# Optimization experiments

Measured on AMD Instinct MI355X. Metric: run time of the kernel, lower is better.

The kernel has to match this reference:

```python
import jax, jax.numpy as jnp
import numpy as np

TOTAL_INSTANCES = 131072
NUM_BAGS = 64
FEATURE_DIM = 512
HIDDEN_DIM = 256


def setup_inputs() -> dict:
    key = jax.random.key(0)
    k1, k2, k3 = jax.random.split(key, 3)
    instance_features = jax.random.normal(k1, (TOTAL_INSTANCES, FEATURE_DIM), dtype=jnp.float32)
    # Equal-sized bags (sum(bag_sizes) == TOTAL_INSTANCES); the reference handles ragged sizes too.
    bag_sizes = jnp.full((NUM_BAGS,), TOTAL_INSTANCES // NUM_BAGS, dtype=jnp.int32)
    W1 = jax.random.normal(k2, (FEATURE_DIM, HIDDEN_DIM), dtype=jnp.float32) * (1.0 / np.sqrt(FEATURE_DIM))
    b1 = jnp.zeros((HIDDEN_DIM,), dtype=jnp.float32)
    W2 = jax.random.normal(k3, (HIDDEN_DIM, 1), dtype=jnp.float32) * (1.0 / np.sqrt(HIDDEN_DIM))
    b2 = jnp.zeros((1,), dtype=jnp.float32)
    return {
        "instance_features": instance_features,
        "bag_sizes": bag_sizes,
        "W1": W1,
        "b1": b1,
        "W2": W2,
        "b2": b2,
    }


def reference(instance_features, bag_sizes, W1, b1, W2, b2):
    # Attention MLP: Linear -> Tanh -> Linear  => scores [T, 1]
    scores = jnp.tanh(instance_features @ W1 + b1) @ W2 + b2
    # Faithful to the original: softmax over dim=0 GLOBALLY across all instances.
    weights = jax.nn.softmax(scores, axis=0)  # [T, 1]
    T = instance_features.shape[0]
    B = bag_sizes.shape[0]
    # Ragged bag membership: instance i belongs to the first bag whose cumulative
    # size exceeds i.
    offsets = jnp.cumsum(bag_sizes)  # [B]
    seg_ids = jnp.searchsorted(offsets, jnp.arange(T), side="right")  # [T]
    # Per-bag weighted sum of instances: [B, feature_dim]
    return jax.ops.segment_sum(instance_features * weights, seg_ids, num_segments=B)
```

## Files before the change

kernel.cpp:

```cpp
#include <hip/hip_runtime.h>

typedef __attribute__((ext_vector_type(8))) short short8;
typedef __attribute__((ext_vector_type(4))) float floatx4;

#define FDIM 512
#define HDIM 256

__device__ __forceinline__ unsigned short f2bf(float f) {
  unsigned int u = __float_as_uint(f);
  u += 0x7fffu + ((u >> 16) & 1u);
  return (unsigned short)(u >> 16);
}

__device__ __forceinline__ short8 pack2(float4 a, float4 b) {
  short8 r;
  r[0] = (short)f2bf(a.x); r[1] = (short)f2bf(a.y);
  r[2] = (short)f2bf(a.z); r[3] = (short)f2bf(a.w);
  r[4] = (short)f2bf(b.x); r[5] = (short)f2bf(b.y);
  r[6] = (short)f2bf(b.z); r[7] = (short)f2bf(b.w);
  return r;
}

__device__ __forceinline__ float fast_tanh(float x) {
  x = fminf(15.0f, fmaxf(-15.0f, x));
  float e = __expf(2.0f * x);
  return (e - 1.0f) / (e + 1.0f);
}

__device__ __forceinline__ void gload_lds16(const void* g, void* l) {
  __builtin_amdgcn_global_load_lds(
      (const __attribute__((address_space(1))) unsigned int*)g,
      (__attribute__((address_space(3))) unsigned int*)l, 16, 0, 0);
}

__global__ void __launch_bounds__(256)
k0_pack_w1(const float* __restrict__ W1, unsigned short* __restrict__ W1B,
           float* __restrict__ out) {
  int tid = threadIdx.x;
  int idx = blockIdx.x * 256 + tid;
  if (blockIdx.x < 128) out[blockIdx.x * 256 + tid] = 0.0f;
  int k = idx >> 8;
  int n = idx & 255;
  int s = k >> 5, r = k & 31, oct = r >> 3, e = r & 7;
  W1B[s * 8192 + oct * 2048 + n * 8 + e] = f2bf(W1[idx]);
}

__global__ void __launch_bounds__(512)
k1_fused(const float* __restrict__ X,
         const unsigned short* __restrict__ W1B,
         const float* __restrict__ b1,
         const float* __restrict__ W2,
         const int* __restrict__ bag_sizes,
         int nbags,
         float* __restrict__ out,
         float* __restrict__ partials) {
  __shared__ __align__(16) unsigned char smem[163840];
  unsigned short* As  = (unsigned short*)smem;
  unsigned short* Bs0 = (unsigned short*)(smem + 131072);
  unsigned short* Bs1 = (unsigned short*)(smem + 147456);
  float* scpart = (float*)(smem + 131072);
  float* es_s   = (float*)(smem + 131072 + 2048);
  float* wsum_s = (float*)(smem + 131072 + 2560);

  const int tid  = threadIdx.x;
  const int wid  = tid >> 6;
  const int lane = tid & 63;
  const int l15  = lane & 15;
  const int l4   = lane >> 4;
  const int wr   = wid >> 2;
  const int wn   = wid & 3;
  const long row0 = (long)blockIdx.x * 128;

  floatx4 acc[4][4];
  #pragma unroll
  for (int m = 0; m < 4; m++)
    #pragma unroll
    for (int n = 0; n < 4; n++)
      acc[m][n] = (floatx4){0.f, 0.f, 0.f, 0.f};

  const int arow = tid >> 2;
  const int aoct = tid & 3;
  const float* xsrc = X + (row0 + arow) * FDIM + aoct * 8;

  float4 va0, va1, vb0, vb1;
  { const float4* pp = (const float4*)xsrc;        va0 = pp[0]; va1 = pp[1]; }
  { const float4* pp = (const float4*)(xsrc + 32); vb0 = pp[0]; vb1 = pp[1]; }
  #pragma unroll
  for (int i = 0; i < 2; ++i)
    gload_lds16(W1B + (i * 512 + tid) * 8, Bs0 + (i * 512 + wid * 64) * 8);

  for (int t = 0; t < 16; ++t) {
    unsigned short* Bcur = (t & 1) ? Bs1 : Bs0;
    {
      int slot = t * 4 + aoct;
      unsigned short* dst = As + (slot * 128 + (arow ^ (slot & 7))) * 8;
      if ((t & 1) == 0) *(short8*)dst = pack2(va0, va1);
      else              *(short8*)dst = pack2(vb0, vb1);
    }
    __syncthreads();
    if (t < 14) {
      const float4* pp = (const float4*)(xsrc + (t + 2) * 32);
      if ((t & 1) == 0) { va0 = pp[0]; va1 = pp[1]; }
      else              { vb0 = pp[0]; vb1 = pp[1]; }
    }
    if (t < 15) {
      unsigned short* Bn = (t & 1) ? Bs0 : Bs1;
      #pragma unroll
      for (int i = 0; i < 2; ++i)
        gload_lds16(W1B + (t + 1) * 8192 + (i * 512 + tid) * 8,
                    Bn + (i * 512 + wid * 64) * 8);
    }
    const int slotc = t * 4 + l4;
    const int gg = slotc & 7;
    short8 af[4];
    #pragma unroll
    for (int m = 0; m < 4; ++m)
      af[m] = *(const short8*)(As + (slotc * 128 + ((wr * 64 + m * 16 + l15) ^ gg)) * 8);
    #pragma unroll
    for (int n = 0; n < 4; ++n) {
      short8 bfr = *(const short8*)(Bcur + (l4 * 256 + wn * 64 + n * 16 + l15) * 8);
      #pragma unroll
      for (int m = 0; m < 4; ++m)
        acc[m][n] = __builtin_amdgcn_mfma_f32_16x16x32_bf16(af[m], bfr, acc[m][n], 0, 0, 0);
    }
  }

  float rowacc[16];
  #pragma unroll
  for (int i = 0; i < 16; i++) rowacc[i] = 0.f;
  #pragma unroll
  for (int n = 0; n < 4; n++) {
    int c = wn * 64 + n * 16 + l15;
    float b1c = b1[c];
    float w2c = W2[c];
    #pragma unroll
    for (int m = 0; m < 4; m++)
      #pragma unroll
      for (int j = 0; j < 4; j++) {
        float h = fast_tanh(acc[m][n][j] + b1c);
        rowacc[m * 4 + j] = fmaf(h, w2c, rowacc[m * 4 + j]);
      }
  }
  #pragma unroll
  for (int i = 0; i < 16; i++) {
    float v = rowacc[i];
    v += __shfl_xor(v, 1, 64);
    v += __shfl_xor(v, 2, 64);
    v += __shfl_xor(v, 4, 64);
    v += __shfl_xor(v, 8, 64);
    rowacc[i] = v;
  }
  if (l15 == 0) {
    #pragma unroll
    for (int m = 0; m < 4; m++)
      #pragma unroll
      for (int j = 0; j < 4; j++)
        scpart[wn * 128 + wr * 64 + m * 16 + l4 * 4 + j] = rowacc[m * 4 + j];
  }
  __syncthreads();

  if (tid < 128) {
    float sv = scpart[0 * 128 + tid] + scpart[1 * 128 + tid] +
               scpart[2 * 128 + tid] + scpart[3 * 128 + tid];
    float ev = __expf(sv);
    es_s[tid] = ev;
    float v = ev;
    v += __shfl_xor(v, 1, 64);
    v += __shfl_xor(v, 2, 64);
    v += __shfl_xor(v, 4, 64);
    v += __shfl_xor(v, 8, 64);
    v += __shfl_xor(v, 16, 64);
    v += __shfl_xor(v, 32, 64);
    if (lane == 0) wsum_s[wid] = v;
  }
  __syncthreads();
  if (tid == 0) partials[blockIdx.x] = wsum_s[0] + wsum_s[1];

  const int s  = tid >> 3;
  const int p  = tid & 7;
  const int gp = s & 7;
  const int fbase = (s >> 2) * 32 + (s & 3) * 8;
  const unsigned short* abase = As + s * 1024;

  int bag = 0; long cum = 0;
  while (bag + 1 < nbags && cum + (long)bag_sizes[bag] <= row0) {
    cum += bag_sizes[bag]; ++bag;
  }
  long bagEnd = cum + (long)bag_sizes[bag];

  int rs = 0;
  while (rs < 128) {
    int se = (int)(bagEnd - row0 < 128 ? bagEnd - row0 : 128);
    float pa[8];
    #pragma unroll
    for (int e = 0; e < 8; ++e) pa[e] = 0.f;
    #pragma unroll
    for (int j = 0; j < 16; ++j) {
      int r = p + 8 * j;
      if (r >= rs && r < se) {
        float w = es_s[r];
        short8 xv = *(const short8*)(abase + ((r ^ gp) * 8));
        const unsigned int* ui = (const unsigned int*)&xv;
        #pragma unroll
        for (int d = 0; d < 4; ++d) {
          float xlo = __uint_as_float(ui[d] << 16);
          float xhi = __uint_as_float(ui[d] & 0xffff0000u);
          pa[2 * d]     = fmaf(xlo, w, pa[2 * d]);
          pa[2 * d + 1] = fmaf(xhi, w, pa[2 * d + 1]);
        }
      }
    }
    #pragma unroll
    for (int e = 0; e < 8; ++e) {
      pa[e] += __shfl_xor(pa[e], 1, 64);
      pa[e] += __shfl_xor(pa[e], 2, 64);
      pa[e] += __shfl_xor(pa[e], 4, 64);
    }
    if (p == 0 && se > rs) {
      float* op = out + (long)bag * FDIM + fbase;
      #pragma unroll
      for (int e = 0; e < 8; ++e) atomicAdd(op + e, pa[e]);
    }
    rs = se;
    if (rs < 128) {
      ++bag;
      if (bag >= nbags) { bagEnd = row0 + 128; bag = nbags - 1; }
      else bagEnd += (long)bag_sizes[bag];
    }
  }
}

__global__ void __launch_bounds__(256)
k2_scale(const float* __restrict__ partials, int nparts, float* __restrict__ out) {
  __shared__ float wred[4];
  int tid = threadIdx.x;
  float sL = 0.f;
  for (int j = tid; j < nparts; j += 256) sL += partials[j];
  #pragma unroll
  for (int m = 1; m < 64; m <<= 1) sL += __shfl_xor(sL, m, 64);
  if ((tid & 63) == 0) wred[tid >> 6] = sL;
  __syncthreads();
  float invZ = 1.0f / (wred[0] + wred[1] + wred[2] + wred[3]);
  int i = blockIdx.x * 256 + tid;
  out[i] = out[i] * invZ;
}

extern "C" void kernel_launch(void* const* d_in, const int* in_sizes, int n_in,
                              void* d_out, int out_size, void* d_ws, size_t ws_size,
                              hipStream_t stream) {
  const float* X         = (const float*)d_in[0];
  const int*   bag_sizes = (const int*)d_in[1];
  const float* W1        = (const float*)d_in[2];
  const float* b1        = (const float*)d_in[3];
  const float* W2        = (const float*)d_in[4];
  float* out = (float*)d_out;

  const int T     = in_sizes[0] / FDIM;
  const int nbags = in_sizes[1];
  const int nblk  = T / 128;

  char* ws = (char*)d_ws;
  unsigned short* W1B = (unsigned short*)ws;
  float* partials = (float*)(ws + 262144);

  hipLaunchKernelGGL(k0_pack_w1, dim3(512), dim3(256), 0, stream, W1, W1B, out);
  hipLaunchKernelGGL(k1_fused, dim3(nblk), dim3(512), 0, stream,
                     X, W1B, b1, W2, bag_sizes, nbags, out, partials);
  hipLaunchKernelGGL(k2_scale, dim3((nbags * FDIM) / 256), dim3(256), 0, stream,
                     partials, nblk, out);
}
```

Measured before the change: 119.0 us.

## Hand-schedule X prefetch and W1 LDS loads with explicit vmcnt waits

Replaces the compiler-generated global loads of X with inline-asm dwordx4 loads and uses explicit s_waitcnt vmcnt counts plus raw s_barrier in place of __syncthreads. Each step waits only for the loads it needs, so X prefetches and W1 global-to-LDS transfers can stay in flight across the barrier. The K loop is also fully unrolled. The cost is a fragile dependence on exact load issue order: a wrong vmcnt value would read stale registers or LDS.

```diff
diff --git a/kernel.cpp b/kernel.cpp
--- a/kernel.cpp
+++ b/kernel.cpp
@@ -12,12 +12,12 @@
   return (unsigned short)(u >> 16);
 }
 
-__device__ __forceinline__ short8 pack2(float4 a, float4 b) {
+__device__ __forceinline__ short8 pack2(floatx4 a, floatx4 b) {
   short8 r;
-  r[0] = (short)f2bf(a.x); r[1] = (short)f2bf(a.y);
-  r[2] = (short)f2bf(a.z); r[3] = (short)f2bf(a.w);
-  r[4] = (short)f2bf(b.x); r[5] = (short)f2bf(b.y);
-  r[6] = (short)f2bf(b.z); r[7] = (short)f2bf(b.w);
+  r[0] = (short)f2bf(a[0]); r[1] = (short)f2bf(a[1]);
+  r[2] = (short)f2bf(a[2]); r[3] = (short)f2bf(a[3]);
+  r[4] = (short)f2bf(b[0]); r[5] = (short)f2bf(b[1]);
+  r[6] = (short)f2bf(b[2]); r[7] = (short)f2bf(b[3]);
   return r;
 }
 
@@ -32,6 +32,14 @@
       (const __attribute__((address_space(1))) unsigned int*)g,
       (__attribute__((address_space(3))) unsigned int*)l, 16, 0, 0);
 }
+
+#define GLOAD_SET(r0, r1, p)                                                   \
+  do {                                                                         \
+    asm volatile("global_load_dwordx4 %0, %1, off"                             \
+                 : "=v"(r0) : "v"(p) : "memory");                              \
+    asm volatile("global_load_dwordx4 %0, %1, off offset:16"                   \
+                 : "=v"(r1) : "v"(p) : "memory");                              \
+  } while (0)
 
 __global__ void __launch_bounds__(256)
 k0_pack_w1(const float* __restrict__ W1, unsigned short* __restrict__ W1B,
@@ -82,33 +90,41 @@
   const int aoct = tid & 3;
   const float* xsrc = X + (row0 + arow) * FDIM + aoct * 8;
 
-  float4 va0, va1, vb0, vb1;
-  { const float4* pp = (const float4*)xsrc;        va0 = pp[0]; va1 = pp[1]; }
-  { const float4* pp = (const float4*)(xsrc + 32); vb0 = pp[0]; vb1 = pp[1]; }
+  floatx4 va0, va1, vb0, vb1;
+
+  GLOAD_SET(va0, va1, xsrc);
   #pragma unroll
   for (int i = 0; i < 2; ++i)
     gload_lds16(W1B + (i * 512 + tid) * 8, Bs0 + (i * 512 + wid * 64) * 8);
-
+  GLOAD_SET(vb0, vb1, xsrc + 32);
+
+  #pragma unroll
   for (int t = 0; t < 16; ++t) {
     unsigned short* Bcur = (t & 1) ? Bs1 : Bs0;
+    if (t < 15) asm volatile("s_waitcnt vmcnt(4)" ::: "memory");
+    else        asm volatile("s_waitcnt vmcnt(2)" ::: "memory");
+    __builtin_amdgcn_sched_barrier(0);
     {
+      short8 a = ((t & 1) == 0) ? pack2(va0, va1) : pack2(vb0, vb1);
       int slot = t * 4 + aoct;
-      unsigned short* dst = As + (slot * 128 + (arow ^ (slot & 7))) * 8;
-      if ((t & 1) == 0) *(short8*)dst = pack2(va0, va1);
-      else              *(short8*)dst = pack2(vb0, vb1);
-    }
-    __syncthreads();
-    if (t < 14) {
-      const float4* pp = (const float4*)(xsrc + (t + 2) * 32);
-      if ((t & 1) == 0) { va0 = pp[0]; va1 = pp[1]; }
-      else              { vb0 = pp[0]; vb1 = pp[1]; }
-    }
+      *(short8*)(As + (slot * 128 + (arow ^ (slot & 7))) * 8) = a;
+    }
+    asm volatile("s_waitcnt lgkmcnt(0)" ::: "memory");
+    if (t < 15) asm volatile("s_waitcnt vmcnt(2)" ::: "memory");
+    else        asm volatile("s_waitcnt vmcnt(0)" ::: "memory");
+    __builtin_amdgcn_sched_barrier(0);
+    __builtin_amdgcn_s_barrier();
     if (t < 15) {
       unsigned short* Bn = (t & 1) ? Bs0 : Bs1;
       #pragma unroll
       for (int i = 0; i < 2; ++i)
         gload_lds16(W1B + (t + 1) * 8192 + (i * 512 + tid) * 8,
                     Bn + (i * 512 + wid * 64) * 8);
+    }
+    if (t < 14) {
+      const float* pp = xsrc + (t + 2) * 32;
+      if ((t & 1) == 0) GLOAD_SET(va0, va1, pp);
+      else              GLOAD_SET(vb0, vb1, pp);
     }
     const int slotc = t * 4 + l4;
     const int gg = slotc & 7;
```

After: 109.4 us. 1.09x faster.

## Replace LDS-tiled block GEMM with independent per-wave 16-row tiles

Applied to the files above, without the earlier changes.

The 512-thread block that staged X and W1 tiles through a large LDS buffer with double-buffered async loads is replaced by waves that each own 16 rows. Each wave keeps its whole bf16 X slice in registers and reads W1 fragments straight from global/L2. Scores, exp and the weighted bag sum are then done with shuffles, with no LDS and no block barriers. The aim is to drop synchronisation and raise occupancy. The cost is rereading W1 from cache for every wave, eight times more partials, and many more atomics, since each wave issues atomics for all 512 features on every pass.

```diff
diff --git a/kernel.cpp b/kernel.cpp
--- a/kernel.cpp
+++ b/kernel.cpp
@@ -10,6 +10,10 @@
   unsigned int u = __float_as_uint(f);
   u += 0x7fffu + ((u >> 16) & 1u);
   return (unsigned short)(u >> 16);
+}
+
+__device__ __forceinline__ float bf2f(unsigned short u) {
+  return __uint_as_float(((unsigned int)u) << 16);
 }
 
 __device__ __forceinline__ short8 pack2(float4 a, float4 b) {
@@ -25,12 +29,6 @@
   x = fminf(15.0f, fmaxf(-15.0f, x));
   float e = __expf(2.0f * x);
   return (e - 1.0f) / (e + 1.0f);
-}
-
-__device__ __forceinline__ void gload_lds16(const void* g, void* l) {
-  __builtin_amdgcn_global_load_lds(
-      (const __attribute__((address_space(1))) unsigned int*)g,
-      (__attribute__((address_space(3))) unsigned int*)l, 16, 0, 0);
 }
 
 __global__ void __launch_bounds__(256)
@@ -45,142 +43,81 @@
   W1B[s * 8192 + oct * 2048 + n * 8 + e] = f2bf(W1[idx]);
 }
 
-__global__ void __launch_bounds__(512)
-k1_fused(const float* __restrict__ X,
-         const unsigned short* __restrict__ W1B,
-         const float* __restrict__ b1,
-         const float* __restrict__ W2,
-         const int* __restrict__ bag_sizes,
-         int nbags,
-         float* __restrict__ out,
-         float* __restrict__ partials) {
-  __shared__ __align__(16) unsigned char smem[163840];
-  unsigned short* As  = (unsigned short*)smem;
-  unsigned short* Bs0 = (unsigned short*)(smem + 131072);
-  unsigned short* Bs1 = (unsigned short*)(smem + 147456);
-  float* scpart = (float*)(smem + 131072);
-  float* es_s   = (float*)(smem + 131072 + 2048);
-  float* wsum_s = (float*)(smem + 131072 + 2560);
-
+__global__ void __launch_bounds__(256)
+k1_mono(const float* __restrict__ X,
+        const unsigned short* __restrict__ W1B,
+        const float* __restrict__ b1,
+        const float* __restrict__ W2,
+        const int* __restrict__ bag_sizes,
+        int nbags,
+        float* __restrict__ out,
+        float* __restrict__ partials) {
   const int tid  = threadIdx.x;
   const int wid  = tid >> 6;
   const int lane = tid & 63;
   const int l15  = lane & 15;
   const int l4   = lane >> 4;
-  const int wr   = wid >> 2;
-  const int wn   = wid & 3;
-  const long row0 = (long)blockIdx.x * 128;
-
-  floatx4 acc[4][4];
-  #pragma unroll
-  for (int m = 0; m < 4; m++)
+  const int wg   = blockIdx.x * 4 + wid;
+  const long row0 = (long)wg * 16;
+
+  floatx4 acc[16];
+  #pragma unroll
+  for (int n = 0; n < 16; ++n) acc[n] = (floatx4){0.f, 0.f, 0.f, 0.f};
+
+  short8 af[16];
+
+  const float* xsrc = X + (row0 + l15) * FDIM + l4 * 8;
+  const unsigned short* bb0 = W1B + l4 * 2048 + l15 * 8;
+
+  #pragma unroll
+  for (int t = 0; t < 16; ++t) {
+    float4 a0 = *(const float4*)(xsrc + t * 32);
+    float4 a1 = *(const float4*)(xsrc + t * 32 + 4);
+    af[t] = pack2(a0, a1);
+    const unsigned short* bb = bb0 + t * 8192;
     #pragma unroll
-    for (int n = 0; n < 4; n++)
-      acc[m][n] = (floatx4){0.f, 0.f, 0.f, 0.f};
-
-  const int arow = tid >> 2;
-  const int aoct = tid & 3;
-  const float* xsrc = X + (row0 + arow) * FDIM + aoct * 8;
-
-  float4 va0, va1, vb0, vb1;
-  { const float4* pp = (const float4*)xsrc;        va0 = pp[0]; va1 = pp[1]; }
-  { const float4* pp = (const float4*)(xsrc + 32); vb0 = pp[0]; vb1 = pp[1]; }
-  #pragma unroll
-  for (int i = 0; i < 2; ++i)
-    gload_lds16(W1B + (i * 512 + tid) * 8, Bs0 + (i * 512 + wid * 64) * 8);
-
-  for (int t = 0; t < 16; ++t) {
-    unsigned short* Bcur = (t & 1) ? Bs1 : Bs0;
-    {
-      int slot = t * 4 + aoct;
-      unsigned short* dst = As + (slot * 128 + (arow ^ (slot & 7))) * 8;
-      if ((t & 1) == 0) *(short8*)dst = pack2(va0, va1);
-      else              *(short8*)dst = pack2(vb0, vb1);
+    for (int n = 0; n < 16; ++n) {
+      short8 bfr = *(const short8*)(bb + n * 128);
+      acc[n] = __builtin_amdgcn_mfma_f32_16x16x32_bf16(af[t], bfr, acc[n], 0, 0, 0);
     }
-    __syncthreads();
-    if (t < 14) {
-      const float4* pp = (const float4*)(xsrc + (t + 2) * 32);
-      if ((t & 1) == 0) { va0 = pp[0]; va1 = pp[1]; }
-      else              { vb0 = pp[0]; vb1 = pp[1]; }
-    }
-    if (t < 15) {
-      unsigned short* Bn = (t & 1) ? Bs0 : Bs1;
-      #pragma unroll
-      for (int i = 0; i < 2; ++i)
-        gload_lds16(W1B + (t + 1) * 8192 + (i * 512 + tid) * 8,
-                    Bn + (i * 512 + wid * 64) * 8);
-    }
-    const int slotc = t * 4 + l4;
-    const int gg = slotc & 7;
-    short8 af[4];
-    #pragma unroll
-    for (int m = 0; m < 4; ++m)
-      af[m] = *(const short8*)(As + (slotc * 128 + ((wr * 64 + m * 16 + l15) ^ gg)) * 8);
-    #pragma unroll
-    for (int n = 0; n < 4; ++n) {
-      short8 bfr = *(const short8*)(Bcur + (l4 * 256 + wn * 64 + n * 16 + l15) * 8);
-      #pragma unroll
-      for (int m = 0; m < 4; ++m)
-        acc[m][n] = __builtin_amdgcn_mfma_f32_16x16x32_bf16(af[m], bfr, acc[m][n], 0, 0, 0);
-    }
-  }
-
-  float rowacc[16];
-  #pragma unroll
-  for (int i = 0; i < 16; i++) rowacc[i] = 0.f;
-  #pragma unroll
-  for (int n = 0; n < 4; n++) {
-    int c = wn * 64 + n * 16 + l15;
+  }
+
+  float rowacc[4] = {0.f, 0.f, 0.f, 0.f};
+  #pragma unroll
+  for (int n = 0; n < 16; ++n) {
+    int c = n * 16 + l15;
     float b1c = b1[c];
     float w2c = W2[c];
     #pragma unroll
-    for (int m = 0; m < 4; m++)
-      #pragma unroll
-      for (int j = 0; j < 4; j++) {
-        float h = fast_tanh(acc[m][n][j] + b1c);
-        rowacc[m * 4 + j] = fmaf(h, w2c, rowacc[m * 4 + j]);
-      }
-  }
-  #pragma unroll
-  for (int i = 0; i < 16; i++) {
-    float v = rowacc[i];
+    for (int j = 0; j < 4; ++j)
+      rowacc[j] = fmaf(fast_tanh(acc[n][j] + b1c), w2c, rowacc[j]);
+  }
+  #pragma unroll
+  for (int j = 0; j < 4; ++j) {
+    float v = rowacc[j];
     v += __shfl_xor(v, 1, 64);
     v += __shfl_xor(v, 2, 64);
     v += __shfl_xor(v, 4, 64);
     v += __shfl_xor(v, 8, 64);
-    rowacc[i] = v;
-  }
-  if (l15 == 0) {
-    #pragma unroll
-    for (int m = 0; m < 4; m++)
-      #pragma unroll
-      for (int j = 0; j < 4; j++)
-        scpart[wn * 128 + wr * 64 + m * 16 + l4 * 4 + j] = rowacc[m * 4 + j];
-  }
-  __syncthreads();
-
-  if (tid < 128) {
-    float sv = scpart[0 * 128 + tid] + scpart[1 * 128 + tid] +
-               scpart[2 * 128 + tid] + scpart[3 * 128 + tid];
-    float ev = __expf(sv);
-    es_s[tid] = ev;
-    float v = ev;
-    v += __shfl_xor(v, 1, 64);
-    v += __shfl_xor(v, 2, 64);
-    v += __shfl_xor(v, 4, 64);
-    v += __shfl_xor(v, 8, 64);
-    v += __shfl_xor(v, 16, 64);
-    v += __shfl_xor(v, 32, 64);
-    if (lane == 0) wsum_s[wid] = v;
-  }
-  __syncthreads();
-  if (tid == 0) partials[blockIdx.x] = wsum_s[0] + wsum_s[1];
-
-  const int s  = tid >> 3;
-  const int p  = tid & 7;
-  const int gp = s & 7;
-  const int fbase = (s >> 2) * 32 + (s & 3) * 8;
-  const unsigned short* abase = As + s * 1024;
+    rowacc[j] = v;
+  }
+  float esj[4];
+  #pragma unroll
+  for (int j = 0; j < 4; ++j) esj[j] = __expf(rowacc[j]);
+
+  float s4 = esj[0] + esj[1] + esj[2] + esj[3];
+  s4 += __shfl_xor(s4, 16, 64);
+  s4 += __shfl_xor(s4, 32, 64);
+  if (lane == 0) partials[wg] = s4;
+
+  int srcl = (l15 >> 2) << 4;
+  float e0 = __shfl(esj[0], srcl, 64);
+  float e1 = __shfl(esj[1], srcl, 64);
+  float e2 = __shfl(esj[2], srcl, 64);
+  float e3 = __shfl(esj[3], srcl, 64);
+  float eA = (l15 & 1) ? e1 : e0;
+  float eB = (l15 & 1) ? e3 : e2;
+  float es_my = (l15 & 2) ? eB : eA;
 
   int bag = 0; long cum = 0;
   while (bag + 1 < nbags && cum + (long)bag_sizes[bag] <= row0) {
@@ -189,42 +126,35 @@
   long bagEnd = cum + (long)bag_sizes[bag];
 
   int rs = 0;
-  while (rs < 128) {
-    int se = (int)(bagEnd - row0 < 128 ? bagEnd - row0 : 128);
-    float pa[8];
+  while (rs < 16) {
+    int se = (int)(bagEnd - row0 < 16 ? bagEnd - row0 : 16);
+    if (se < rs) se = rs;
+    float wme = (l15 >= rs && l15 < se) ? es_my : 0.f;
+    float* obase = out + (long)bag * FDIM;
+    bool doatom = (l15 == 0) && (se > rs);
     #pragma unroll
-    for (int e = 0; e < 8; ++e) pa[e] = 0.f;
-    #pragma unroll
-    for (int j = 0; j < 16; ++j) {
-      int r = p + 8 * j;
-      if (r >= rs && r < se) {
-        float w = es_s[r];
-        short8 xv = *(const short8*)(abase + ((r ^ gp) * 8));
-        const unsigned int* ui = (const unsigned int*)&xv;
+    for (int t = 0; t < 16; ++t) {
+      float p[8];
+      #pragma unroll
+      for (int e = 0; e < 8; ++e)
+        p[e] = bf2f((unsigned short)af[t][e]) * wme;
+      #pragma unroll
+      for (int e = 0; e < 8; ++e) {
+        p[e] += __shfl_xor(p[e], 1, 64);
+        p[e] += __shfl_xor(p[e], 2, 64);
+        p[e] += __shfl_xor(p[e], 4, 64);
+        p[e] += __shfl_xor(p[e], 8, 64);
+      }
+      if (doatom) {
+        float* op = obase + t * 32 + l4 * 8;
         #pragma unroll
-        for (int d = 0; d < 4; ++d) {
-          float xlo = __uint_as_float(ui[d] << 16);
-          float xhi = __uint_as_float(ui[d] & 0xffff0000u);
-          pa[2 * d]     = fmaf(xlo, w, pa[2 * d]);
-          pa[2 * d + 1] = fmaf(xhi, w, pa[2 * d + 1]);
-        }
+        for (int e = 0; e < 8; ++e) atomicAdd(op + e, p[e]);
       }
     }
-    #pragma unroll
-    for (int e = 0; e < 8; ++e) {
-      pa[e] += __shfl_xor(pa[e], 1, 64);
-      pa[e] += __shfl_xor(pa[e], 2, 64);
-      pa[e] += __shfl_xor(pa[e], 4, 64);
-    }
-    if (p == 0 && se > rs) {
-      float* op = out + (long)bag * FDIM + fbase;
-      #pragma unroll
-      for (int e = 0; e < 8; ++e) atomicAdd(op + e, pa[e]);
-    }
     rs = se;
-    if (rs < 128) {
+    if (rs < 16) {
       ++bag;
-      if (bag >= nbags) { bagEnd = row0 + 128; bag = nbags - 1; }
+      if (bag >= nbags) { bagEnd = row0 + 16; bag = nbags - 1; }
       else bagEnd += (long)bag_sizes[bag];
     }
   }
@@ -257,15 +187,16 @@
 
   const int T     = in_sizes[0] / FDIM;
   const int nbags = in_sizes[1];
-  const int nblk  = T / 128;
+  const int nblk  = T / 64;
+  const int nwave = T / 16;
 
   char* ws = (char*)d_ws;
   unsigned short* W1B = (unsigned short*)ws;
   float* partials = (float*)(ws + 262144);
 
   hipLaunchKernelGGL(k0_pack_w1, dim3(512), dim3(256), 0, stream, W1, W1B, out);
-  hipLaunchKernelGGL(k1_fused, dim3(nblk), dim3(512), 0, stream,
+  hipLaunchKernelGGL(k1_mono, dim3(nblk), dim3(256), 0, stream,
                      X, W1B, b1, W2, bag_sizes, nbags, out, partials);
   hipLaunchKernelGGL(k2_scale, dim3((nbags * FDIM) / 256), dim3(256), 0, stream,
-                     partials, nblk, out);
-}
+                     partials, nwave, out);
+}
```

Measured after the change: 355.7 us. 199% more time.
